# Kernel optimization log

Hardware: AMD Instinct MI355X
Metric: run time of the kernel (lower is better)

The kernel has to match this reference:

```python
import jax, jax.numpy as jnp
import numpy as np

T, H, I = 4096, 4096, 11008  # tokens, hidden, intermediate


def setup_inputs() -> dict:
    key = jax.random.key(0)
    k = jax.random.split(key, 6)
    # int8-range quantized activations and weights (stored as int32 for jax matmul)
    x_q = jax.random.randint(k[0], (T, H), -127, 128).astype(jnp.int32)
    w_gate_up = jax.random.randint(k[1], (2 * I, H), -127, 128).astype(jnp.int32)
    w_down = jax.random.randint(k[2], (H, I), -127, 128).astype(jnp.int32)
    # per-token dynamic input scale, per-output-channel weight scales
    x_scale = jax.random.uniform(k[3], (T,), jnp.float32, 1e-4, 2e-2)
    s_w_gate_up = jax.random.uniform(k[4], (2 * I,), jnp.float32, 1e-4, 2e-2)
    s_w_down = jax.random.uniform(k[5], (H,), jnp.float32, 1e-4, 2e-2)
    return {"x_q": x_q, "x_scale": x_scale, "w_gate_up": w_gate_up,
            "s_w_gate_up": s_w_gate_up, "w_down": w_down, "s_w_down": s_w_down}


def reference(x_q, x_scale, w_gate_up, s_w_gate_up, w_down, s_w_down):
    # --- gate_up_proj: W8A8 int8 GEMM + dequant (per-token x per-channel scales) ---
    gu_i32 = jnp.matmul(x_q, w_gate_up.T)                                   # [T, 2I] int32 accum
    gu = gu_i32.astype(jnp.float32) * x_scale[:, None] * s_w_gate_up[None, :]
    gate, up = gu[:, :I], gu[:, I:]
    # --- SiluAndMulQuant: fused SiLU(gate)*up + per-token dynamic requant to int8 ---
    y = jax.nn.silu(gate) * up                                              # [T, I] fp
    s2 = jnp.maximum(jnp.max(jnp.abs(y), axis=-1), 1e-8) / 127.0            # [T] new dynamic scale
    y_q = jnp.clip(jnp.round(y / s2[:, None]), -128.0, 127.0).astype(jnp.int32)
    # --- down_proj: W8A8 int8 GEMM + dequant ---
    out_i32 = jnp.matmul(y_q, w_down.T)                                     # [T, H] int32 accum
    out = out_i32.astype(jnp.float32) * s2[:, None] * s_w_down[None, :]
    return out
```

## Files before the change

### kernel.cpp

```cpp
#include <hip/hip_runtime.h>
#include <cstdint>
#include <cstddef>

#define T_DIM 4096
#define H_DIM 4096
#define I_DIM 11008

typedef int v4i  __attribute__((ext_vector_type(4)));
typedef int v16i __attribute__((ext_vector_type(16)));

__device__ __forceinline__ void async_copy16(const void* g, void* l) {
  __builtin_amdgcn_global_load_lds(
      (const __attribute__((address_space(1))) void*)g,
      (__attribute__((address_space(3))) void*)l, 16, 0, 0);
}

__device__ __forceinline__ void stage_tile(const int8_t* src, size_t ld,
                                           char* ldsbase, int wave, int lane) {
#pragma unroll
  for (int q = 0; q < 2; ++q) {
    int seg = q * 4 + wave;
    int r = seg * 16 + (lane >> 2);
    int p = lane & 3;
    int c = p ^ ((r >> 1) & 3);
    const int8_t* g = src + (size_t)r * ld + (size_t)c * 16;
    char* lp = ldsbase + seg * 1024;
    async_copy16((const void*)g, (void*)lp);
  }
}

__device__ __forceinline__ v4i frag32(const char* ldsbase, int rowbase,
                                      int kc2, int lane) {
  int r = rowbase + (lane & 31);
  int c = (kc2 + (lane >> 5)) ^ ((r >> 1) & 3);
  return *(const v4i*)(ldsbase + r * 64 + c * 16);
}

__global__ void pack_i8(const int4* __restrict__ src, v4i* __restrict__ dst, int n16) {
  int stride = gridDim.x * blockDim.x;
  for (int i = blockIdx.x * blockDim.x + threadIdx.x; i < n16; i += stride) {
    int4 a = src[4 * i + 0], b = src[4 * i + 1];
    int4 c = src[4 * i + 2], d = src[4 * i + 3];
    v4i o;
    o[0] = (a.x & 255) | ((a.y & 255) << 8) | ((a.z & 255) << 16) | (a.w << 24);
    o[1] = (b.x & 255) | ((b.y & 255) << 8) | ((b.z & 255) << 16) | (b.w << 24);
    o[2] = (c.x & 255) | ((c.y & 255) << 8) | ((c.z & 255) << 16) | (c.w << 24);
    o[3] = (d.x & 255) | ((d.y & 255) << 8) | ((d.z & 255) << 16) | (d.w << 24);
    dst[i] = o;
  }
}

__global__ void zero_u32(unsigned* __restrict__ p, int n) {
  int i = blockIdx.x * blockDim.x + threadIdx.x;
  if (i < n) p[i] = 0u;
}

__global__ __launch_bounds__(256, 2)
void gemm1_silu(const int8_t* __restrict__ x8,
                const int8_t* __restrict__ wgu8,
                const float* __restrict__ x_scale,
                const float* __restrict__ s_wgu,
                float* __restrict__ y,
                unsigned* __restrict__ rowmax) {
  __shared__ __align__(16) char lds[49152];

  const int tid = threadIdx.x;
  const int wave = tid >> 6, lane = tid & 63;
  const int wm = wave >> 1, wn = wave & 1;
  const int m0 = blockIdx.y * 128;
  const int n0 = blockIdx.x * 128;

  v16i vzero;
#pragma unroll
  for (int e = 0; e < 16; e++) vzero[e] = 0;
  v16i accg[2][2], accu[2][2];
#pragma unroll
  for (int i = 0; i < 2; i++)
#pragma unroll
    for (int j = 0; j < 2; j++) { accg[i][j] = vzero; accu[i][j] = vzero; }

  const int8_t* Ab  = x8 + (size_t)m0 * H_DIM;
  const int8_t* Bgb = wgu8 + (size_t)n0 * H_DIM;
  const int8_t* Bub = wgu8 + ((size_t)I_DIM + (size_t)n0) * H_DIM;

  stage_tile(Ab, H_DIM, lds, wave, lane);
  stage_tile(Bgb, H_DIM, lds + 8192, wave, lane);
  stage_tile(Bub, H_DIM, lds + 16384, wave, lane);

  int cur = 0;
  for (int k0 = 0; k0 < H_DIM; k0 += 64) {
    __syncthreads();
    char* buf = lds + cur * 24576;
    if (k0 + 64 < H_DIM) {
      char* nb = lds + (cur ^ 1) * 24576;
      stage_tile(Ab + k0 + 64, H_DIM, nb, wave, lane);
      stage_tile(Bgb + k0 + 64, H_DIM, nb + 8192, wave, lane);
      stage_tile(Bub + k0 + 64, H_DIM, nb + 16384, wave, lane);
    }
#pragma unroll
    for (int ks = 0; ks < 2; ++ks) {
      v4i a[2], bg[2], bu[2];
#pragma unroll
      for (int i = 0; i < 2; i++) a[i]  = frag32(buf,         wm * 64 + i * 32, ks * 2, lane);
#pragma unroll
      for (int j = 0; j < 2; j++) bg[j] = frag32(buf + 8192,  wn * 64 + j * 32, ks * 2, lane);
#pragma unroll
      for (int j = 0; j < 2; j++) bu[j] = frag32(buf + 16384, wn * 64 + j * 32, ks * 2, lane);
#pragma unroll
      for (int i = 0; i < 2; i++)
#pragma unroll
        for (int j = 0; j < 2; j++) {
          accg[i][j] = __builtin_amdgcn_mfma_i32_32x32x32_i8(a[i], bg[j], accg[i][j], 0, 0, 0);
          accu[i][j] = __builtin_amdgcn_mfma_i32_32x32x32_i8(a[i], bu[j], accu[i][j], 0, 0, 0);
        }
    }
    cur ^= 1;
  }

  const int lc = lane & 31;
  const int lh = lane >> 5;
#pragma unroll
  for (int i = 0; i < 2; i++) {
#pragma unroll
    for (int r = 0; r < 16; r++) {
      const int gr = m0 + wm * 64 + i * 32 + (r & 3) + 8 * (r >> 2) + 4 * lh;
      const float sx = x_scale[gr];
      float vmax = 0.f;
#pragma unroll
      for (int j = 0; j < 2; j++) {
        const int gc = n0 + wn * 64 + j * 32 + lc;
        float g = (float)accg[i][j][r] * sx * s_wgu[gc];
        float u = (float)accu[i][j][r] * sx * s_wgu[I_DIM + gc];
        float yv = (g / (1.f + expf(-g))) * u;
        y[(size_t)gr * I_DIM + gc] = yv;
        vmax = fmaxf(vmax, fabsf(yv));
      }
#pragma unroll
      for (int off = 1; off < 32; off <<= 1)
        vmax = fmaxf(vmax, __shfl_xor(vmax, off, 64));
      if (lc == 0) atomicMax(&rowmax[gr], __float_as_uint(vmax));
    }
  }
}

__global__ void quantize_y(const float* __restrict__ y,
                           const unsigned* __restrict__ rowmax,
                           v4i* __restrict__ yq) {
  size_t i = (size_t)blockIdx.x * blockDim.x + threadIdx.x;
  if (i >= (size_t)T_DIM * I_DIM / 16) return;
  size_t base = i * 16;
  int row = (int)(base / I_DIM);
  float inv = 127.f / fmaxf(__uint_as_float(rowmax[row]), 1e-8f);
  const float4* p = (const float4*)(y + base);
  v4i o;
#pragma unroll
  for (int q = 0; q < 4; q++) {
    float4 v = p[q];
    int b0 = (int)fminf(127.f, fmaxf(-128.f, rintf(v.x * inv)));
    int b1 = (int)fminf(127.f, fmaxf(-128.f, rintf(v.y * inv)));
    int b2 = (int)fminf(127.f, fmaxf(-128.f, rintf(v.z * inv)));
    int b3 = (int)fminf(127.f, fmaxf(-128.f, rintf(v.w * inv)));
    o[q] = (b0 & 255) | ((b1 & 255) << 8) | ((b2 & 255) << 16) | (b3 << 24);
  }
  yq[i] = o;
}

__global__ __launch_bounds__(256, 3)
void gemm2_scaled(const int8_t* __restrict__ yq8,
                  const int8_t* __restrict__ wd8,
                  const unsigned* __restrict__ rowmax,
                  const float* __restrict__ s_wd,
                  float* __restrict__ out) {
  __shared__ __align__(16) char lds[32768];

  const int tid = threadIdx.x;
  const int wave = tid >> 6, lane = tid & 63;
  const int wm = wave >> 1, wn = wave & 1;
  const int m0 = blockIdx.y * 128;
  const int n0 = blockIdx.x * 128;

  v16i vzero;
#pragma unroll
  for (int e = 0; e < 16; e++) vzero[e] = 0;
  v16i acc[2][2];
#pragma unroll
  for (int i = 0; i < 2; i++)
#pragma unroll
    for (int j = 0; j < 2; j++) acc[i][j] = vzero;

  const int8_t* Ab = yq8 + (size_t)m0 * I_DIM;
  const int8_t* Bb = wd8 + (size_t)n0 * I_DIM;

  stage_tile(Ab, I_DIM, lds, wave, lane);
  stage_tile(Bb, I_DIM, lds + 8192, wave, lane);

  int cur = 0;
  for (int k0 = 0; k0 < I_DIM; k0 += 64) {
    __syncthreads();
    char* buf = lds + cur * 16384;
    if (k0 + 64 < I_DIM) {
      char* nb = lds + (cur ^ 1) * 16384;
      stage_tile(Ab + k0 + 64, I_DIM, nb, wave, lane);
      stage_tile(Bb + k0 + 64, I_DIM, nb + 8192, wave, lane);
    }
#pragma unroll
    for (int ks = 0; ks < 2; ++ks) {
      v4i a[2], b[2];
#pragma unroll
      for (int i = 0; i < 2; i++) a[i] = frag32(buf,        wm * 64 + i * 32, ks * 2, lane);
#pragma unroll
      for (int j = 0; j < 2; j++) b[j] = frag32(buf + 8192, wn * 64 + j * 32, ks * 2, lane);
#pragma unroll
      for (int i = 0; i < 2; i++)
#pragma unroll
        for (int j = 0; j < 2; j++)
          acc[i][j] = __builtin_amdgcn_mfma_i32_32x32x32_i8(a[i], b[j], acc[i][j], 0, 0, 0);
    }
    cur ^= 1;
  }

  const int lc = lane & 31;
  const int lh = lane >> 5;
#pragma unroll
  for (int i = 0; i < 2; i++) {
#pragma unroll
    for (int r = 0; r < 16; r++) {
      const int gr = m0 + wm * 64 + i * 32 + (r & 3) + 8 * (r >> 2) + 4 * lh;
      const float s2 = fmaxf(__uint_as_float(rowmax[gr]), 1e-8f) / 127.f;
#pragma unroll
      for (int j = 0; j < 2; j++) {
        const int gc = n0 + wn * 64 + j * 32 + lc;
        out[(size_t)gr * H_DIM + gc] = (float)acc[i][j][r] * s2 * s_wd[gc];
      }
    }
  }
}

extern "C" void kernel_launch(void* const* d_in, const int* in_sizes, int n_in,
                              void* d_out, int out_size, void* d_ws, size_t ws_size,
                              hipStream_t stream) {
  const int*   x_q     = (const int*)d_in[0];
  const float* x_scale = (const float*)d_in[1];
  const int*   w_gu    = (const int*)d_in[2];
  const float* s_wgu   = (const float*)d_in[3];
  const int*   w_d     = (const int*)d_in[4];
  const float* s_wd    = (const float*)d_in[5];
  float* out = (float*)d_out;

  char* ws = (char*)d_ws;
  const size_t SZ_X8   = (size_t)T_DIM * H_DIM;
  const size_t SZ_WGU8 = (size_t)2 * I_DIM * H_DIM;
  const size_t SZ_WD8  = (size_t)H_DIM * I_DIM;
  const size_t SZ_Y    = (size_t)T_DIM * I_DIM * 4;
  const size_t SZ_YQ   = (size_t)T_DIM * I_DIM;

  int8_t*   x8     = (int8_t*)ws;
  int8_t*   wgu8   = (int8_t*)(ws + SZ_X8);
  int8_t*   wd8    = (int8_t*)(ws + SZ_X8 + SZ_WGU8);
  float*    y      = (float*)(ws + SZ_X8 + SZ_WGU8 + SZ_WD8);
  int8_t*   yq8    = (int8_t*)(ws + SZ_X8 + SZ_WGU8 + SZ_WD8 + SZ_Y);
  unsigned* rowmax = (unsigned*)(ws + SZ_X8 + SZ_WGU8 + SZ_WD8 + SZ_Y + SZ_YQ);

  pack_i8<<<dim3(4096), dim3(256), 0, stream>>>((const int4*)x_q,  (v4i*)x8,   (int)(SZ_X8 / 16));
  pack_i8<<<dim3(4096), dim3(256), 0, stream>>>((const int4*)w_gu, (v4i*)wgu8, (int)(SZ_WGU8 / 16));
  pack_i8<<<dim3(4096), dim3(256), 0, stream>>>((const int4*)w_d,  (v4i*)wd8,  (int)(SZ_WD8 / 16));
  zero_u32<<<dim3(16), dim3(256), 0, stream>>>(rowmax, T_DIM);

  gemm1_silu<<<dim3(I_DIM / 128, T_DIM / 128), dim3(256), 0, stream>>>(
      x8, wgu8, x_scale, s_wgu, y, rowmax);

  quantize_y<<<dim3((unsigned)(((size_t)T_DIM * I_DIM / 16 + 255) / 256)), dim3(256), 0, stream>>>(
      y, rowmax, (v4i*)yq8);

  gemm2_scaled<<<dim3(H_DIM / 128, T_DIM / 128), dim3(256), 0, stream>>>(
      yq8, wd8, rowmax, s_wd, out);
}
```

Baseline: 1.528 ms.

## Use 512-thread blocks with K=128 single-buffered tiles in both GEMMs

After: 1.566 ms. +2.5%, slower.

```diff
diff --git a/kernel.cpp b/kernel.cpp
--- a/kernel.cpp
+++ b/kernel.cpp
@@ -15,25 +15,24 @@
       (__attribute__((address_space(3))) void*)l, 16, 0, 0);
 }
 
-__device__ __forceinline__ void stage_tile(const int8_t* src, size_t ld,
-                                           char* ldsbase, int wave, int lane) {
+__device__ __forceinline__ void stage_tile128(const int8_t* src, size_t ld,
+                                              char* ldsbase, int wave, int lane) {
 #pragma unroll
   for (int q = 0; q < 2; ++q) {
-    int seg = q * 4 + wave;
-    int r = seg * 16 + (lane >> 2);
-    int p = lane & 3;
-    int c = p ^ ((r >> 1) & 3);
+    int r = wave * 16 + q * 8 + (lane >> 3);
+    int p = lane & 7;
+    int c = p ^ (r & 7);
     const int8_t* g = src + (size_t)r * ld + (size_t)c * 16;
-    char* lp = ldsbase + seg * 1024;
+    char* lp = ldsbase + (wave * 16 + q * 8) * 128;
     async_copy16((const void*)g, (void*)lp);
   }
 }
 
-__device__ __forceinline__ v4i frag32(const char* ldsbase, int rowbase,
-                                      int kc2, int lane) {
+__device__ __forceinline__ v4i frag128(const char* tile, int rowbase,
+                                       int kc, int lane) {
   int r = rowbase + (lane & 31);
-  int c = (kc2 + (lane >> 5)) ^ ((r >> 1) & 3);
-  return *(const v4i*)(ldsbase + r * 64 + c * 16);
+  int c = (kc + (lane >> 5)) ^ (r & 7);
+  return *(const v4i*)(tile + r * 128 + c * 16);
 }
 
 __global__ void pack_i8(const int4* __restrict__ src, v4i* __restrict__ dst, int n16) {
@@ -55,7 +54,7 @@
   if (i < n) p[i] = 0u;
 }
 
-__global__ __launch_bounds__(256, 2)
+__global__ __launch_bounds__(512, 4)
 void gemm1_silu(const int8_t* __restrict__ x8,
                 const int8_t* __restrict__ wgu8,
                 const float* __restrict__ x_scale,
@@ -63,78 +62,63 @@
                 float* __restrict__ y,
                 unsigned* __restrict__ rowmax) {
   __shared__ __align__(16) char lds[49152];
+  char* ldsA  = lds;
+  char* ldsBg = lds + 16384;
+  char* ldsBu = lds + 32768;
 
   const int tid = threadIdx.x;
   const int wave = tid >> 6, lane = tid & 63;
-  const int wm = wave >> 1, wn = wave & 1;
+  const int wm = wave >> 2;
+  const int wn = wave & 3;
   const int m0 = blockIdx.y * 128;
   const int n0 = blockIdx.x * 128;
 
-  v16i vzero;
-#pragma unroll
-  for (int e = 0; e < 16; e++) vzero[e] = 0;
-  v16i accg[2][2], accu[2][2];
-#pragma unroll
-  for (int i = 0; i < 2; i++)
-#pragma unroll
-    for (int j = 0; j < 2; j++) { accg[i][j] = vzero; accu[i][j] = vzero; }
+  v16i accg[2], accu[2];
+#pragma unroll
+  for (int i = 0; i < 2; i++) {
+#pragma unroll
+    for (int e = 0; e < 16; e++) { accg[i][e] = 0; accu[i][e] = 0; }
+  }
 
   const int8_t* Ab  = x8 + (size_t)m0 * H_DIM;
   const int8_t* Bgb = wgu8 + (size_t)n0 * H_DIM;
   const int8_t* Bub = wgu8 + ((size_t)I_DIM + (size_t)n0) * H_DIM;
 
-  stage_tile(Ab, H_DIM, lds, wave, lane);
-  stage_tile(Bgb, H_DIM, lds + 8192, wave, lane);
-  stage_tile(Bub, H_DIM, lds + 16384, wave, lane);
-
-  int cur = 0;
-  for (int k0 = 0; k0 < H_DIM; k0 += 64) {
-    __syncthreads();
-    char* buf = lds + cur * 24576;
-    if (k0 + 64 < H_DIM) {
-      char* nb = lds + (cur ^ 1) * 24576;
-      stage_tile(Ab + k0 + 64, H_DIM, nb, wave, lane);
-      stage_tile(Bgb + k0 + 64, H_DIM, nb + 8192, wave, lane);
-      stage_tile(Bub + k0 + 64, H_DIM, nb + 16384, wave, lane);
-    }
-#pragma unroll
-    for (int ks = 0; ks < 2; ++ks) {
-      v4i a[2], bg[2], bu[2];
-#pragma unroll
-      for (int i = 0; i < 2; i++) a[i]  = frag32(buf,         wm * 64 + i * 32, ks * 2, lane);
-#pragma unroll
-      for (int j = 0; j < 2; j++) bg[j] = frag32(buf + 8192,  wn * 64 + j * 32, ks * 2, lane);
-#pragma unroll
-      for (int j = 0; j < 2; j++) bu[j] = frag32(buf + 16384, wn * 64 + j * 32, ks * 2, lane);
-#pragma unroll
-      for (int i = 0; i < 2; i++)
-#pragma unroll
-        for (int j = 0; j < 2; j++) {
-          accg[i][j] = __builtin_amdgcn_mfma_i32_32x32x32_i8(a[i], bg[j], accg[i][j], 0, 0, 0);
-          accu[i][j] = __builtin_amdgcn_mfma_i32_32x32x32_i8(a[i], bu[j], accu[i][j], 0, 0, 0);
-        }
-    }
-    cur ^= 1;
+  for (int k0 = 0; k0 < H_DIM; k0 += 128) {
+    __syncthreads();
+    stage_tile128(Ab + k0, H_DIM, ldsA, wave, lane);
+    stage_tile128(Bgb + k0, H_DIM, ldsBg, wave, lane);
+    stage_tile128(Bub + k0, H_DIM, ldsBu, wave, lane);
+    __syncthreads();
+#pragma unroll
+    for (int ks = 0; ks < 4; ++ks) {
+      v4i a0 = frag128(ldsA,  wm * 64,      ks * 2, lane);
+      v4i a1 = frag128(ldsA,  wm * 64 + 32, ks * 2, lane);
+      v4i bg = frag128(ldsBg, wn * 32,      ks * 2, lane);
+      v4i bu = frag128(ldsBu, wn * 32,      ks * 2, lane);
+      accg[0] = __builtin_amdgcn_mfma_i32_32x32x32_i8(a0, bg, accg[0], 0, 0, 0);
+      accu[0] = __builtin_amdgcn_mfma_i32_32x32x32_i8(a0, bu, accu[0], 0, 0, 0);
+      accg[1] = __builtin_amdgcn_mfma_i32_32x32x32_i8(a1, bg, accg[1], 0, 0, 0);
+      accu[1] = __builtin_amdgcn_mfma_i32_32x32x32_i8(a1, bu, accu[1], 0, 0, 0);
+    }
   }
 
   const int lc = lane & 31;
   const int lh = lane >> 5;
+  const int gc = n0 + wn * 32 + lc;
+  const float swg = s_wgu[gc];
+  const float swu = s_wgu[I_DIM + gc];
 #pragma unroll
   for (int i = 0; i < 2; i++) {
 #pragma unroll
     for (int r = 0; r < 16; r++) {
       const int gr = m0 + wm * 64 + i * 32 + (r & 3) + 8 * (r >> 2) + 4 * lh;
       const float sx = x_scale[gr];
-      float vmax = 0.f;
-#pragma unroll
-      for (int j = 0; j < 2; j++) {
-        const int gc = n0 + wn * 64 + j * 32 + lc;
-        float g = (float)accg[i][j][r] * sx * s_wgu[gc];
-        float u = (float)accu[i][j][r] * sx * s_wgu[I_DIM + gc];
-        float yv = (g / (1.f + expf(-g))) * u;
-        y[(size_t)gr * I_DIM + gc] = yv;
-        vmax = fmaxf(vmax, fabsf(yv));
-      }
+      float g = (float)accg[i][r] * sx * swg;
+      float u = (float)accu[i][r] * sx * swu;
+      float yv = (g / (1.f + expf(-g))) * u;
+      y[(size_t)gr * I_DIM + gc] = yv;
+      float vmax = fabsf(yv);
 #pragma unroll
       for (int off = 1; off < 32; off <<= 1)
         vmax = fmaxf(vmax, __shfl_xor(vmax, off, 64));
@@ -165,73 +149,58 @@
   yq[i] = o;
 }
 
-__global__ __launch_bounds__(256, 3)
+__global__ __launch_bounds__(512, 4)
 void gemm2_scaled(const int8_t* __restrict__ yq8,
                   const int8_t* __restrict__ wd8,
                   const unsigned* __restrict__ rowmax,
                   const float* __restrict__ s_wd,
                   float* __restrict__ out) {
   __shared__ __align__(16) char lds[32768];
+  char* ldsA = lds;
+  char* ldsB = lds + 16384;
 
   const int tid = threadIdx.x;
   const int wave = tid >> 6, lane = tid & 63;
-  const int wm = wave >> 1, wn = wave & 1;
+  const int wm = wave >> 2;
+  const int wn = wave & 3;
   const int m0 = blockIdx.y * 128;
   const int n0 = blockIdx.x * 128;
 
-  v16i vzero;
-#pragma unroll
-  for (int e = 0; e < 16; e++) vzero[e] = 0;
-  v16i acc[2][2];
+  v16i acc[2];
 #pragma unroll
   for (int i = 0; i < 2; i++)
 #pragma unroll
-    for (int j = 0; j < 2; j++) acc[i][j] = vzero;
+    for (int e = 0; e < 16; e++) acc[i][e] = 0;
 
   const int8_t* Ab = yq8 + (size_t)m0 * I_DIM;
   const int8_t* Bb = wd8 + (size_t)n0 * I_DIM;
 
-  stage_tile(Ab, I_DIM, lds, wave, lane);
-  stage_tile(Bb, I_DIM, lds + 8192, wave, lane);
-
-  int cur = 0;
-  for (int k0 = 0; k0 < I_DIM; k0 += 64) {
-    __syncthreads();
-    char* buf = lds + cur * 16384;
-    if (k0 + 64 < I_DIM) {
-      char* nb = lds + (cur ^ 1) * 16384;
-      stage_tile(Ab + k0 + 64, I_DIM, nb, wave, lane);
-      stage_tile(Bb + k0 + 64, I_DIM, nb + 8192, wave, lane);
-    }
-#pragma unroll
-    for (int ks = 0; ks < 2; ++ks) {
-      v4i a[2], b[2];
-#pragma unroll
-      for (int i = 0; i < 2; i++) a[i] = frag32(buf,        wm * 64 + i * 32, ks * 2, lane);
-#pragma unroll
-      for (int j = 0; j < 2; j++) b[j] = frag32(buf + 8192, wn * 64 + j * 32, ks * 2, lane);
-#pragma unroll
-      for (int i = 0; i < 2; i++)
-#pragma unroll
-        for (int j = 0; j < 2; j++)
-          acc[i][j] = __builtin_amdgcn_mfma_i32_32x32x32_i8(a[i], b[j], acc[i][j], 0, 0, 0);
-    }
-    cur ^= 1;
+  for (int k0 = 0; k0 < I_DIM; k0 += 128) {
+    __syncthreads();
+    stage_tile128(Ab + k0, I_DIM, ldsA, wave, lane);
+    stage_tile128(Bb + k0, I_DIM, ldsB, wave, lane);
+    __syncthreads();
+#pragma unroll
+    for (int ks = 0; ks < 4; ++ks) {
+      v4i a0 = frag128(ldsA, wm * 64,      ks * 2, lane);
+      v4i a1 = frag128(ldsA, wm * 64 + 32, ks * 2, lane);
+      v4i b  = frag128(ldsB, wn * 32,      ks * 2, lane);
+      acc[0] = __builtin_amdgcn_mfma_i32_32x32x32_i8(a0, b, acc[0], 0, 0, 0);
+      acc[1] = __builtin_amdgcn_mfma_i32_32x32x32_i8(a1, b, acc[1], 0, 0, 0);
+    }
   }
 
   const int lc = lane & 31;
   const int lh = lane >> 5;
+  const int gc = n0 + wn * 32 + lc;
+  const float swd = s_wd[gc];
 #pragma unroll
   for (int i = 0; i < 2; i++) {
 #pragma unroll
     for (int r = 0; r < 16; r++) {
       const int gr = m0 + wm * 64 + i * 32 + (r & 3) + 8 * (r >> 2) + 4 * lh;
       const float s2 = fmaxf(__uint_as_float(rowmax[gr]), 1e-8f) / 127.f;
-#pragma unroll
-      for (int j = 0; j < 2; j++) {
-        const int gc = n0 + wn * 64 + j * 32 + lc;
-        out[(size_t)gr * H_DIM + gc] = (float)acc[i][j][r] * s2 * s_wd[gc];
-      }
+      out[(size_t)gr * H_DIM + gc] = (float)acc[i][r] * s2 * swd;
     }
   }
 }
@@ -266,12 +235,12 @@
   pack_i8<<<dim3(4096), dim3(256), 0, stream>>>((const int4*)w_d,  (v4i*)wd8,  (int)(SZ_WD8 / 16));
   zero_u32<<<dim3(16), dim3(256), 0, stream>>>(rowmax, T_DIM);
 
-  gemm1_silu<<<dim3(I_DIM / 128, T_DIM / 128), dim3(256), 0, stream>>>(
+  gemm1_silu<<<dim3(I_DIM / 128, T_DIM / 128), dim3(512), 0, stream>>>(
       x8, wgu8, x_scale, s_wgu, y, rowmax);
 
   quantize_y<<<dim3((unsigned)(((size_t)T_DIM * I_DIM / 16 + 255) / 256)), dim3(256), 0, stream>>>(
       y, rowmax, (v4i*)yq8);
 
-  gemm2_scaled<<<dim3(H_DIM / 128, T_DIM / 128), dim3(256), 0, stream>>>(
+  gemm2_scaled<<<dim3(H_DIM / 128, T_DIM / 128), dim3(512), 0, stream>>>(
       yq8, wd8, rowmax, s_wd, out);
 }
```
